# Optimization experiments

Hardware: AMD Instinct MI355X
Metric: run time of the kernel (lower is better)

Reference implementation:

```python
import jax, jax.numpy as jnp
import numpy as np

B, T, D = 4, 4096, 1024
H, K, V = 16, 64, 64
EPS = 1e-6


def setup_inputs() -> dict:
    key = jax.random.key(0)
    ks = jax.random.split(key, 7)
    s = 0.02
    return {
        "x": jax.random.normal(ks[0], (B, T, D), dtype=jnp.float32),
        "norm_w": jnp.ones((D,), dtype=jnp.float32),
        "Wk": jax.random.normal(ks[1], (H * K, D), dtype=jnp.float32) * s,
        "Wv": jax.random.normal(ks[2], (H * V, D), dtype=jnp.float32) * s,
        "Wo": jax.random.normal(ks[3], (D, H * V), dtype=jnp.float32) * s,
        "Wb": jax.random.normal(ks[4], (H, D), dtype=jnp.float32) * s,
        "bb": jnp.full((H,), -2.0, dtype=jnp.float32),
        "Wg": jax.random.normal(ks[5], (H, D), dtype=jnp.float32) * s,
        "bg": jnp.full((H,), 2.0, dtype=jnp.float32),
    }


def reference(x, norm_w, Wk, Wv, Wo, Wb, bb, Wg, bg):
    # RMSNorm
    rms = jnp.sqrt(jnp.mean(x * x, axis=-1, keepdims=True) + EPS)
    xn = x / rms * norm_w  # [B,T,D]

    k = (xn @ Wk.T).reshape(B, T, H, K)
    v = (xn @ Wv.T).reshape(B, T, H, V)
    # L2-normalize keys (F.normalize, eps=1e-12)
    kn = jnp.linalg.norm(k, axis=-1, keepdims=True)
    k = k / jnp.maximum(kn, 1e-12)

    beta = jax.nn.sigmoid(xn @ Wb.T + bb)  # [B,T,H]
    g = jax.nn.sigmoid(xn @ Wg.T + bg)     # [B,T,H]

    # time-major for scan
    k_t = jnp.transpose(k, (1, 0, 2, 3))       # [T,B,H,K]
    v_t = jnpp = jnp.transpose(v, (1, 0, 2, 3))  # [T,B,H,V]
    b_t = jnp.transpose(beta, (1, 0, 2))       # [T,B,H]
    g_t = jnp.transpose(g, (1, 0, 2))          # [T,B,H]

    state0 = jnp.zeros((B, H, K, V), dtype=jnp.float32)

    def step(state, inp):
        kt, vt, bt, gt = inp  # [B,H,K],[B,H,V],[B,H],[B,H]
        pred = jnp.einsum('bhkv,bhk->bhv', state, kt)
        err = vt - pred
        state = gt[..., None, None] * state + bt[..., None, None] * (kt[..., :, None] * err[..., None, :])
        out_t = jnp.einsum('bhkv,bhk->bhv', state, kt)
        return state, out_t

    final_state, out = jax.lax.scan(step, state0, (k_t, v_t, b_t, g_t))
    out = jnp.transpose(out, (1, 0, 2, 3)).reshape(B, T, H * V)  # [B,T,H*V]
    y = x + out @ Wo.T
    return y
```

## Files before the change

kernel.cpp:

```cpp
#include <hip/hip_runtime.h>
#include <stdint.h>

#define B_ 4
#define T_ 4096
#define D_ 1024
#define H_ 16
#define NPAD 2304
#define ROWS (B_*T_)

typedef __bf16 bf16x8 __attribute__((ext_vector_type(8)));
typedef float  f32x4  __attribute__((ext_vector_type(4)));
typedef unsigned short u16;
typedef u16 u16x8 __attribute__((ext_vector_type(8)));
typedef u16 u16x4 __attribute__((ext_vector_type(4)));

__device__ __forceinline__ float bf2f(u16 u){
  union { unsigned int i; float f; } x; x.i = ((unsigned int)u) << 16; return x.f;
}
__device__ __forceinline__ u16 f2bf(float f){
  union { float f; unsigned int i; } x; x.f = f;
  unsigned int r = x.i + 0x7fffu + ((x.i >> 16) & 1u);
  return (u16)(r >> 16);
}
__device__ __forceinline__ bf16x8 as_bf(u16x8 v){ union{u16x8 u; bf16x8 b;} x; x.u = v; return x.b; }

__device__ __forceinline__ void gload_lds16(const u16* g, u16* l){
  __builtin_amdgcn_global_load_lds(
      (const __attribute__((address_space(1))) unsigned int*)g,
      (__attribute__((address_space(3))) unsigned int*)l, 16, 0, 0);
}

__global__ __launch_bounds__(256) void prep_w(
    const float* __restrict__ Wk, const float* __restrict__ Wv,
    const float* __restrict__ Wb, const float* __restrict__ Wg,
    const float* __restrict__ Wo, u16* __restrict__ Wcomb, u16* __restrict__ Wob)
{
  long i = (long)blockIdx.x * 256 + threadIdx.x;
  const long tot1 = (long)NPAD * D_;
  if (i < tot1) {
    long n = i >> 10, d = i & 1023;
    float v;
    if      (n < 1024) v = Wk[n * 1024 + d];
    else if (n < 2048) v = Wv[(n - 1024) * 1024 + d];
    else if (n < 2064) v = Wb[(n - 2048) * 1024 + d];
    else if (n < 2080) v = Wg[(n - 2064) * 1024 + d];
    else               v = 0.f;
    Wcomb[i] = f2bf(v);
  } else {
    long j = i - tot1;
    Wob[j] = f2bf(Wo[j]);
  }
}

__global__ __launch_bounds__(256) void rmsnorm_k(
    const float* __restrict__ x, const float* __restrict__ w, u16* __restrict__ xn)
{
  long row = blockIdx.x;
  int tid = threadIdx.x;
  int l = tid & 63, wv = tid >> 6;
  f32x4 v = ((const f32x4*)(x + row * D_))[tid];
  float ss = v[0]*v[0] + v[1]*v[1] + v[2]*v[2] + v[3]*v[3];
  #pragma unroll
  for (int m = 1; m < 64; m <<= 1) ss += __shfl_xor(ss, m, 64);
  __shared__ float red[4];
  if (l == 0) red[wv] = ss;
  __syncthreads();
  float tot = red[0] + red[1] + red[2] + red[3];
  float inv = rsqrtf(tot * (1.f / (float)D_) + 1e-6f);
  f32x4 wv4 = ((const f32x4*)w)[tid];
  u16x4 o;
  o[0] = f2bf(v[0] * inv * wv4[0]);
  o[1] = f2bf(v[1] * inv * wv4[1]);
  o[2] = f2bf(v[2] * inv * wv4[2]);
  o[3] = f2bf(v[3] * inv * wv4[3]);
  ((u16x4*)(xn + row * D_))[tid] = o;
}

extern __shared__ f32x4 lds_dyn[];

template<int RESID, int OUTF32>
__global__ __launch_bounds__(512, 2) void gemm256(
    const u16* __restrict__ A, const u16* __restrict__ Bm,
    u16* __restrict__ Cb, float* __restrict__ Cf, const float* __restrict__ resid,
    int M, int N, int Kd)
{
  const int tid = threadIdx.x;
  const int w = tid >> 6, l = tid & 63;
  const int lm = l & 15, lq = l >> 4;
  const int wm = w >> 2, wn = w & 3;

  unsigned gx = gridDim.x;
  unsigned bid = blockIdx.y * gx + blockIdx.x;
  unsigned nwg = gx * gridDim.y;
  unsigned cpx = nwg >> 3;
  unsigned swz = (bid & 7) * cpx + (bid >> 3);
  const long bm0 = (long)(swz / gx) * 256;
  const long bn0 = (long)(swz % gx) * 256;

  char* lds = (char*)lds_dyn;

  int rowS[2];
  #pragma unroll
  for (int r = 0; r < 2; ++r) rowS[r] = r*128 + w*16 + (l >> 2);
  const int colS = ((l & 3) ^ ((l >> 3) & 3)) * 8;

  auto STAGE = [&](int t, int q){
    char* base = lds + q*32768;
    long k0 = (long)t * 32;
    #pragma unroll
    for (int r = 0; r < 2; ++r)
      gload_lds16(A + (bm0 + rowS[r])*(long)Kd + k0 + colS,
                  (u16*)(base + (r*512 + w*64)*16));
    #pragma unroll
    for (int r = 0; r < 2; ++r)
      gload_lds16(Bm + (bn0 + rowS[r])*(long)Kd + k0 + colS,
                  (u16*)(base + 16384 + (r*512 + w*64)*16));
  };

  const unsigned soff = (unsigned)(lq ^ ((lm >> 1) & 3)) << 4;

  f32x4 acc[8][4];
  #pragma unroll
  for (int i = 0; i < 8; ++i)
    #pragma unroll
    for (int j = 0; j < 4; ++j) acc[i][j] = f32x4{0.f,0.f,0.f,0.f};

  const int NT = Kd >> 5;
  STAGE(0, 0);
  STAGE(1, 1);
  STAGE(2, 2);

  for (int t = 0; t < NT; ++t) {
    int q  = t & 3;
    int qn = (t + 3) & 3;
    int tn = (t + 3 < NT) ? (t + 3) : (NT - 1);

    asm volatile("s_waitcnt vmcnt(8)" ::: "memory");
    __builtin_amdgcn_s_barrier();
    asm volatile("" ::: "memory");

    STAGE(tn, qn);

    const char* Ab = lds + q*32768;
    const char* Bb = Ab + 16384;

    bf16x8 bfr[4], afr[8];
    #pragma unroll
    for (int nf = 0; nf < 4; ++nf) {
      int rr = wn*64 + nf*16 + lm;
      bfr[nf] = *(const bf16x8*)(Bb + rr*64 + soff);
    }
    #pragma unroll
    for (int mf = 0; mf < 8; ++mf) {
      int rr = wm*128 + mf*16 + lm;
      afr[mf] = *(const bf16x8*)(Ab + rr*64 + soff);
    }

    __builtin_amdgcn_s_setprio(1);
    #pragma unroll
    for (int mf = 0; mf < 8; ++mf)
      #pragma unroll
      for (int nf = 0; nf < 4; ++nf)
        acc[mf][nf] = __builtin_amdgcn_mfma_f32_16x16x32_bf16(afr[mf], bfr[nf], acc[mf][nf], 0, 0, 0);
    __builtin_amdgcn_s_setprio(0);
  }

  #pragma unroll
  for (int mf = 0; mf < 8; ++mf) {
    #pragma unroll
    for (int r = 0; r < 4; ++r) {
      long m = bm0 + wm*128 + mf*16 + lq*4 + r;
      #pragma unroll
      for (int nf = 0; nf < 4; ++nf) {
        long n = bn0 + wn*64 + nf*16 + lm;
        float val = acc[mf][nf][r];
        if (RESID) val += resid[m * N + n];
        if (OUTF32) Cf[m * N + n] = val;
        else        Cb[m * N + n] = f2bf(val);
      }
    }
  }
}

template<int RESID, int OUTF32>
__global__ __launch_bounds__(256) void gemm_nt(
    const u16* __restrict__ A, const u16* __restrict__ Bm,
    u16* __restrict__ Cb, float* __restrict__ Cf, const float* __restrict__ resid,
    int M, int N, int Kd)
{
  __shared__ __align__(16) u16 Als[128 * 32];
  __shared__ __align__(16) u16 Bls[128 * 32];
  const int tid = threadIdx.x;
  const int w = tid >> 6, l = tid & 63;
  const int wr = w >> 1, wc = w & 1;
  const int lm = l & 15, lq = l >> 4;

  unsigned bid = blockIdx.y * gridDim.x + blockIdx.x;
  unsigned nwg = gridDim.x * gridDim.y;
  unsigned cpx = nwg >> 3;
  unsigned swz = (bid & 7) * cpx + (bid >> 3);
  const long bm0 = (long)(swz / gridDim.x) * 128;
  const long bn0 = (long)(swz % gridDim.x) * 128;

  f32x4 zero4 = {0.f, 0.f, 0.f, 0.f};
  f32x4 acc[4][4];
  #pragma unroll
  for (int i = 0; i < 4; i++)
    #pragma unroll
    for (int j = 0; j < 4; j++) acc[i][j] = zero4;

  for (int kk = 0; kk < Kd; kk += 32) {
    __syncthreads();
    #pragma unroll
    for (int it = 0; it < 2; it++) {
      int c = tid + it * 256;
      int r = c >> 2, kb = c & 3;
      const u16* ga = A  + (bm0 + r) * Kd + kk + kb * 8;
      const u16* gb = Bm + (bn0 + r) * Kd + kk + kb * 8;
      gload_lds16(ga, Als + (it * 256 + w * 64) * 8);
      gload_lds16(gb, Bls + (it * 256 + w * 64) * 8);
    }
    __syncthreads();
    bf16x8 af[4], bfr[4];
    #pragma unroll
    for (int f = 0; f < 4; f++)
      af[f] = *(const bf16x8*)(Als + (wr * 64 + f * 16 + lm) * 32 + lq * 8);
    #pragma unroll
    for (int f = 0; f < 4; f++)
      bfr[f] = *(const bf16x8*)(Bls + (wc * 64 + f * 16 + lm) * 32 + lq * 8);
    #pragma unroll
    for (int i = 0; i < 4; i++)
      #pragma unroll
      for (int j = 0; j < 4; j++)
        acc[i][j] = __builtin_amdgcn_mfma_f32_16x16x32_bf16(af[i], bfr[j], acc[i][j], 0, 0, 0);
  }

  #pragma unroll
  for (int i = 0; i < 4; i++) {
    #pragma unroll
    for (int r = 0; r < 4; r++) {
      long m = bm0 + wr * 64 + i * 16 + lq * 4 + r;
      #pragma unroll
      for (int j = 0; j < 4; j++) {
        long n = bn0 + wc * 64 + j * 16 + lm;
        float val = acc[i][j][r];
        if (RESID) val += resid[m * N + n];
        if (OUTF32) Cf[m * N + n] = val;
        else        Cb[m * N + n] = f2bf(val);
      }
    }
  }
}

__global__ __launch_bounds__(256) void sigmoid_bg(
    const u16* __restrict__ kv, const float* __restrict__ bb, const float* __restrict__ bg,
    float* __restrict__ bArr, float* __restrict__ gArr)
{
  int idx = blockIdx.x * 256 + threadIdx.x;
  int row = idx >> 5, c = idx & 31;
  int h = c & 15;
  float val = bf2f(kv[(long)row * NPAD + 2048 + c]) + ((c < 16) ? bb[h] : bg[h]);
  float s = 1.f / (1.f + expf(-val));
  long b = row >> 12, t = row & 4095;
  float* dst = (c < 16) ? bArr : gArr;
  dst[(b * H_ + h) * (long)T_ + t] = s;
}

__device__ __forceinline__ void mm64(const u16* Ab, const u16* Bb,
                                     int lm, int lq, int wr, int wc, f32x4 acc[2][2])
{
  #pragma unroll
  for (int ks = 0; ks < 2; ++ks) {
    bf16x8 af[2], bfr[2];
    #pragma unroll
    for (int mi = 0; mi < 2; ++mi)
      af[mi] = *(const bf16x8*)(Ab + (wr*32 + mi*16 + lm)*72 + ks*32 + lq*8);
    #pragma unroll
    for (int ni = 0; ni < 2; ++ni)
      bfr[ni] = *(const bf16x8*)(Bb + (wc*32 + ni*16 + lm)*72 + ks*32 + lq*8);
    #pragma unroll
    for (int mi = 0; mi < 2; ++mi)
      #pragma unroll
      for (int ni = 0; ni < 2; ++ni)
        acc[mi][ni] = __builtin_amdgcn_mfma_f32_16x16x32_bf16(af[mi], bfr[ni], acc[mi][ni], 0, 0, 0);
  }
}

__global__ __launch_bounds__(256) void chunk1(
    u16* __restrict__ kv, const float* __restrict__ bArr, const float* __restrict__ gArr,
    u16* __restrict__ p1buf, u16* __restrict__ r1buf)
{
  __shared__ __align__(16) u16 Kb[64*72];
  __shared__ __align__(16) u16 Utb[128*72];
  __shared__ __align__(16) u16 LpI[64*72];
  __shared__ __align__(16) u16 Abf[64*72];
  __shared__ __align__(16) u16 Adb[4*16*24];
  __shared__ float nrm2LS[64];
  __shared__ float aLS[64], ainvLS[64], bLS[64], bapLS[64];
  __shared__ float aCsh;

  const int tid = threadIdx.x;
  const int w = tid >> 6, l = tid & 63;
  const int lm = l & 15, lq = l >> 4;
  const int wr = w >> 1, wc = w & 1;
  const int bh = blockIdx.x & 63, ch = blockIdx.x >> 6;
  const int b = bh >> 4, h = bh & 15;

  const u16* kbase = kv + ((long)b*T_ + ch*64)*NPAD + h*64;
  const u16* vbase = kbase + 1024;

  #pragma unroll
  for (int it = 0; it < 2; ++it) {
    int c = tid + it*256;
    int r = c >> 3, seg = (c & 7)*8;
    *(u16x8*)(Kb  + r*72 + seg) = *(const u16x8*)(kbase + (long)r*NPAD + seg);
    *(u16x8*)(Utb + r*72 + seg) = *(const u16x8*)(vbase + (long)r*NPAD + seg);
  }
  #pragma unroll
  for (int z = 0; z < 8; ++z) {
    int idx = tid + z*256;
    int rr = idx >> 5, wd = idx & 31;
    ((unsigned int*)(Utb + (64 + rr)*72))[wd] = 0u;
  }
  if (tid < 64) {
    float gv = gArr[(long)bh*T_ + ch*64 + tid];
    float bv = bArr[(long)bh*T_ + ch*64 + tid];
    float av = gv;
    #pragma unroll
    for (int off = 1; off < 64; off <<= 1) {
      float o = __shfl_up(av, off, 64);
      if (tid >= off) av *= o;
    }
    float ap = __shfl_up(av, 1, 64);
    if (tid == 0) ap = 1.f;
    float aC = __shfl(av, 63, 64);
    aLS[tid] = av; ainvLS[tid] = 1.f/av; bLS[tid] = bv; bapLS[tid] = bv*ap;
    if (tid == 0) aCsh = aC;
  }
  __syncthreads();

  f32x4 gf[2][2];
  #pragma unroll
  for (int mi = 0; mi < 2; ++mi)
    #pragma unroll
    for (int ni = 0; ni < 2; ++ni) gf[mi][ni] = f32x4{0.f,0.f,0.f,0.f};
  mm64(Kb, Kb, lm, lq, wr, wc, gf);

  #pragma unroll
  for (int mi = 0; mi < 2; ++mi)
    #pragma unroll
    for (int ni = 0; ni < 2; ++ni)
      #pragma unroll
      for (int r = 0; r < 4; ++r) {
        int row = wr*32 + mi*16 + lq*4 + r, col = wc*32 + ni*16 + lm;
        if (row == col) nrm2LS[row] = gf[mi][ni][r];
      }
  __syncthreads();
  if (tid < 64) {
    float nv = 1.f / fmaxf(sqrtf(nrm2LS[tid]), 1e-12f);
    aLS[tid] *= nv; ainvLS[tid] *= nv; bapLS[tid] *= nv;
  }
  __syncthreads();

  float wv_[4][2][4];
  #pragma unroll
  for (int bi = 0; bi < 4; ++bi)
    #pragma unroll
    for (int ni = 0; ni < 2; ++ni) {
      int col = w*32 + ni*16 + lm;
      #pragma unroll
      for (int r = 0; r < 4; ++r) {
        int row = bi*16 + lq*4 + r;
        float sv = (col < 64) ? bf2f(Utb[row*72 + col]) : bf2f(Kb[row*72 + (col - 64)]);
        float coef = (col < 64) ? bLS[row] : bapLS[row];
        wv_[bi][ni][r] = coef * sv;
      }
    }

  #pragma unroll
  for (int mi = 0; mi < 2; ++mi)
    #pragma unroll
    for (int ni = 0; ni < 2; ++ni)
      #pragma unroll
      for (int r = 0; r < 4; ++r) {
        int row = wr*32 + mi*16 + lq*4 + r, col = wc*32 + ni*16 + lm;
        float gvl = gf[mi][ni][r];
        int rb = row >> 4, cb = col >> 4;
        Abf[row*72 + col] = f2bf((rb > cb) ? bapLS[row]*ainvLS[col]*gvl : 0.f);
        if (rb == cb)
          Adb[rb*384 + (row & 15)*24 + (col & 15)] =
              f2bf(((col & 15) < (row & 15)) ? bapLS[row]*ainvLS[col]*gvl : 0.f);
        LpI[row*72 + col] = f2bf((col < row) ? aLS[row]*ainvLS[col]*gvl
                                             : ((col == row) ? 1.f : 0.f));
      }
  __syncthreads();

  #pragma unroll
  for (int bi = 0; bi < 4; ++bi) {
    if (bi > 0) {
      f32x4 corr[2] = { f32x4{0.f,0.f,0.f,0.f}, f32x4{0.f,0.f,0.f,0.f} };
      const int nks = (bi*16 + 31) >> 5;
      #pragma unroll
      for (int ks = 0; ks < 2; ++ks) {
        if (ks < nks) {
          bf16x8 afr = *(const bf16x8*)(Abf + (bi*16 + lm)*72 + ks*32 + lq*8);
          #pragma unroll
          for (int ni = 0; ni < 2; ++ni) {
            bf16x8 bfr = *(const bf16x8*)(Utb + (w*32 + ni*16 + lm)*72 + ks*32 + lq*8);
            corr[ni] = __builtin_amdgcn_mfma_f32_16x16x32_bf16(afr, bfr, corr[ni], 0, 0, 0);
          }
        }
      }
      #pragma unroll
      for (int ni = 0; ni < 2; ++ni)
        #pragma unroll
        for (int r = 0; r < 4; ++r) wv_[bi][ni][r] -= corr[ni][r];
    }
    u16x8 ad0[4], ad1[4];
    #pragma unroll
    for (int r = 0; r < 4; ++r) {
      ad0[r] = *(const u16x8*)(Adb + bi*384 + (lq*4 + r)*24);
      ad1[r] = *(const u16x8*)(Adb + bi*384 + (lq*4 + r)*24 + 8);
    }
    #pragma unroll
    for (int i = 0; i < 16; ++i) {
      int src = ((i >> 2) << 4) | lm;
      float u0 = __shfl(wv_[bi][0][i & 3], src, 64);
      float u1 = __shfl(wv_[bi][1][i & 3], src, 64);
      #pragma unroll
      for (int r = 0; r < 4; ++r) {
        float ad = bf2f((i < 8) ? ad0[r][i] : ad1[r][i - 8]);
        wv_[bi][0][r] = fmaf(-ad, u0, wv_[bi][0][r]);
        wv_[bi][1][r] = fmaf(-ad, u1, wv_[bi][1][r]);
      }
    }
    #pragma unroll
    for (int ni = 0; ni < 2; ++ni) {
      int col = w*32 + ni*16 + lm;
      #pragma unroll
      for (int r = 0; r < 4; ++r)
        Utb[col*72 + bi*16 + lq*4 + r] = f2bf(wv_[bi][ni][r]);
    }
  }
  __syncthreads();

  const long pr_base = (((long)bh*64 + ch)*64);
  u16* qdst = kv + ((long)b*T_ + ch*64)*NPAD + h*64;
  u16* mdst = qdst + 1024;
  f32x4 acc[2][2];

  #pragma unroll
  for (int mi = 0; mi < 2; ++mi)
    #pragma unroll
    for (int ni = 0; ni < 2; ++ni) acc[mi][ni] = f32x4{0.f,0.f,0.f,0.f};
  mm64(Utb, LpI, lm, lq, wr, wc, acc);
  #pragma unroll
  for (int mi = 0; mi < 2; ++mi)
    #pragma unroll
    for (int ni = 0; ni < 2; ++ni)
      #pragma unroll
      for (int r = 0; r < 4; ++r) {
        int row = wr*32 + mi*16 + lq*4 + r, col = wc*32 + ni*16 + lm;
        p1buf[(pr_base + row)*64 + col] = f2bf(acc[mi][ni][r]);
      }

  #pragma unroll
  for (int mi = 0; mi < 2; ++mi)
    #pragma unroll
    for (int ni = 0; ni < 2; ++ni) acc[mi][ni] = f32x4{0.f,0.f,0.f,0.f};
  mm64(LpI, Utb + 64*72, lm, lq, wr, wc, acc);
  #pragma unroll
  for (int mi = 0; mi < 2; ++mi)
    #pragma unroll
    for (int ni = 0; ni < 2; ++ni)
      #pragma unroll
      for (int r = 0; r < 4; ++r) {
        int row = wr*32 + mi*16 + lq*4 + r, col = wc*32 + ni*16 + lm;
        float val = aLS[row]*bf2f(Kb[row*72 + col]) - acc[mi][ni][r];
        qdst[(long)row*NPAD + col] = f2bf(val);
      }

  {
    int s = tid & 63, kk0 = (tid >> 6) * 16;
    float coef = aCsh * ainvLS[s];
    #pragma unroll
    for (int j = 0; j < 16; ++j)
      Abf[(kk0 + j)*72 + s] = f2bf(coef * bf2f(Kb[s*72 + kk0 + j]));
  }
  __syncthreads();

  #pragma unroll
  for (int mi = 0; mi < 2; ++mi)
    #pragma unroll
    for (int ni = 0; ni < 2; ++ni) acc[mi][ni] = f32x4{0.f,0.f,0.f,0.f};
  mm64(Utb, Abf, lm, lq, wr, wc, acc);
  #pragma unroll
  for (int mi = 0; mi < 2; ++mi)
    #pragma unroll
    for (int ni = 0; ni < 2; ++ni)
      #pragma unroll
      for (int r = 0; r < 4; ++r) {
        int row = wr*32 + mi*16 + lq*4 + r, col = wc*32 + ni*16 + lm;
        r1buf[(pr_base + row)*64 + col] = f2bf(acc[mi][ni][r]);
      }

  #pragma unroll
  for (int mi = 0; mi < 2; ++mi)
    #pragma unroll
    for (int ni = 0; ni < 2; ++ni) acc[mi][ni] = f32x4{0.f,0.f,0.f,0.f};
  mm64(Abf, Utb + 64*72, lm, lq, wr, wc, acc);
  #pragma unroll
  for (int mi = 0; mi < 2; ++mi)
    #pragma unroll
    for (int ni = 0; ni < 2; ++ni)
      #pragma unroll
      for (int r = 0; r < 4; ++r) {
        int row = wr*32 + mi*16 + lq*4 + r, col = wc*32 + ni*16 + lm;
        float val = ((row == col) ? aCsh : 0.f) - acc[mi][ni][r];
        mdst[(long)row*NPAD + col] = f2bf(val);
      }
}

struct PF { u16x8 qf0, qf1, mf0, mf1; u16 p1[4]; u16 r1[4]; };

__global__ __launch_bounds__(256) void chunk2(
    const u16* __restrict__ kv, const u16* __restrict__ p1buf, const u16* __restrict__ r1buf,
    u16* __restrict__ outb)
{
  __shared__ __align__(16) u16 Zb[16*72];
  __shared__ __align__(16) u16 ot[64*24];
  const int tid = threadIdx.x;
  const int wcv = tid >> 6, l = tid & 63;
  const int lm = l & 15, lq = l >> 4;
  const int bh = blockIdx.x & 63, vg = blockIdx.x >> 6;
  const int b = bh >> 4, h = bh & 15;

  for (int idx = tid; idx < 16*72/2; idx += 256) ((unsigned int*)Zb)[idx] = 0u;

  const u16* pbase = p1buf + (long)bh*64*4096;
  const u16* rbase = r1buf + (long)bh*64*4096;

  auto LOADPF = [&](int ch, PF& p){
    long rq = ((long)b*T_ + ch*64 + wcv*16 + lm)*NPAD + h*64 + lq*8;
    p.qf0 = *(const u16x8*)(kv + rq);
    p.qf1 = *(const u16x8*)(kv + rq + 32);
    p.mf0 = *(const u16x8*)(kv + rq + 1024);
    p.mf1 = *(const u16x8*)(kv + rq + 1024 + 32);
    #pragma unroll
    for (int r = 0; r < 4; ++r) {
      long pv = (long)ch*4096 + (vg*16 + lq*4 + r)*64 + wcv*16 + lm;
      p.p1[r] = pbase[pv];
      p.r1[r] = rbase[pv];
    }
  };

  PF A, Bp;
  LOADPF(0, A);
  __syncthreads();

  auto STEP = [&](int ch, PF& use, PF& pre){
    bf16x8 za0 = *(const bf16x8*)(Zb + lm*72 + lq*8);
    bf16x8 za1 = *(const bf16x8*)(Zb + lm*72 + 32 + lq*8);
    if (ch < 63) LOADPF(ch + 1, pre);
    f32x4 accO = { bf2f(use.p1[0]), bf2f(use.p1[1]), bf2f(use.p1[2]), bf2f(use.p1[3]) };
    accO = __builtin_amdgcn_mfma_f32_16x16x32_bf16(za0, as_bf(use.qf0), accO, 0, 0, 0);
    accO = __builtin_amdgcn_mfma_f32_16x16x32_bf16(za1, as_bf(use.qf1), accO, 0, 0, 0);
    f32x4 accS = { bf2f(use.r1[0]), bf2f(use.r1[1]), bf2f(use.r1[2]), bf2f(use.r1[3]) };
    accS = __builtin_amdgcn_mfma_f32_16x16x32_bf16(za0, as_bf(use.mf0), accS, 0, 0, 0);
    accS = __builtin_amdgcn_mfma_f32_16x16x32_bf16(za1, as_bf(use.mf1), accS, 0, 0, 0);
    #pragma unroll
    for (int r = 0; r < 4; ++r) ot[(wcv*16 + lm)*24 + lq*4 + r] = f2bf(accO[r]);
    __syncthreads();
    #pragma unroll
    for (int r = 0; r < 4; ++r) Zb[(lq*4 + r)*72 + wcv*16 + lm] = f2bf(accS[r]);
    {
      int i2 = tid >> 2, q4 = tid & 3;
      u16x4 ov = *(const u16x4*)(ot + i2*24 + q4*4);
      *(u16x4*)(outb + ((long)b*T_ + ch*64 + i2)*D_ + h*64 + vg*16 + q4*4) = ov;
    }
    __syncthreads();
  };

  for (int c2 = 0; c2 < 32; ++c2) {
    STEP(2*c2,     A, Bp);
    STEP(2*c2 + 1, Bp, A);
  }
}

extern "C" void kernel_launch(void* const* d_in, const int* in_sizes, int n_in,
                              void* d_out, int out_size, void* d_ws, size_t ws_size,
                              hipStream_t stream) {
  const float* x     = (const float*)d_in[0];
  const float* normw = (const float*)d_in[1];
  const float* Wk    = (const float*)d_in[2];
  const float* Wv    = (const float*)d_in[3];
  const float* Wo    = (const float*)d_in[4];
  const float* Wb    = (const float*)d_in[5];
  const float* bb    = (const float*)d_in[6];
  const float* Wg    = (const float*)d_in[7];
  const float* bg    = (const float*)d_in[8];
  float* y = (float*)d_out;

  char* ws = (char*)d_ws;
  u16* xn    = (u16*)ws;   ws += (long)ROWS * D_ * 2;
  u16* Wcomb = (u16*)ws;   ws += (long)NPAD * D_ * 2;
  u16* Wob   = (u16*)ws;   ws += (long)D_ * D_ * 2;
  u16* kvb   = (u16*)ws;   ws += (long)ROWS * NPAD * 2;
  float* bA  = (float*)ws; ws += (long)B_ * H_ * T_ * 4;
  float* gA  = (float*)ws; ws += (long)B_ * H_ * T_ * 4;
  u16* outb  = (u16*)ws;   ws += (long)ROWS * D_ * 2;
  u16* r1b   = (u16*)ws;   ws += (long)64 * 64 * 4096 * 2;

  const int LDSB = 4 * 32768;
  bool big = true;
  if (hipFuncSetAttribute(reinterpret_cast<const void*>(gemm256<0,0>),
        hipFuncAttributeMaxDynamicSharedMemorySize, LDSB) != hipSuccess) big = false;
  if (hipFuncSetAttribute(reinterpret_cast<const void*>(gemm256<1,1>),
        hipFuncAttributeMaxDynamicSharedMemorySize, LDSB) != hipSuccess) big = false;

  const long prep_total = (long)NPAD * D_ + (long)D_ * D_;
  prep_w<<<dim3((unsigned)(prep_total / 256)), dim3(256), 0, stream>>>(
      Wk, Wv, Wb, Wg, Wo, Wcomb, Wob);
  rmsnorm_k<<<dim3(ROWS), dim3(256), 0, stream>>>(x, normw, xn);
  if (big)
    gemm256<0, 0><<<dim3(NPAD / 256, ROWS / 256), dim3(512), LDSB, stream>>>(
        xn, Wcomb, kvb, (float*)nullptr, (const float*)nullptr, ROWS, NPAD, D_);
  else
    gemm_nt<0, 0><<<dim3(NPAD / 128, ROWS / 128), dim3(256), 0, stream>>>(
        xn, Wcomb, kvb, (float*)nullptr, (const float*)nullptr, ROWS, NPAD, D_);
  sigmoid_bg<<<dim3(ROWS * 32 / 256), dim3(256), 0, stream>>>(kvb, bb, bg, bA, gA);
  chunk1<<<dim3(4096), dim3(256), 0, stream>>>(kvb, bA, gA, xn, r1b);
  chunk2<<<dim3(256), dim3(256), 0, stream>>>(kvb, xn, r1b, outb);
  if (big)
    gemm256<1, 1><<<dim3(D_ / 256, ROWS / 256), dim3(512), LDSB, stream>>>(
        outb, Wob, (u16*)nullptr, y, x, ROWS, D_, D_);
  else
    gemm_nt<1, 1><<<dim3(D_ / 128, ROWS / 128), dim3(256), 0, stream>>>(
        outb, Wob, (u16*)nullptr, y, x, ROWS, D_, D_);
}
```

Before: 323.3 us.

## Restructure 256x256 GEMM into 8-phase ping-pong pipeline with K=64 tiles

Replaces the 4-stage K=32 GEMM main loop with a double-buffered K=64 scheme. Each iteration is split into four MFMA quadrant phases, and the global-to-LDS loads for the next tiles are spread across those phases. Barriers, s_waitcnt and sched_barrier control the interleaving, and the LDS layout uses a new 128-byte row XOR swizzle. The goal is better overlap of memory loads, LDS reads and MFMA work in both projection GEMMs, at the cost of more barriers and a fragile hand-scheduled wait count.

```diff
diff --git a/kernel.cpp b/kernel.cpp
--- a/kernel.cpp
+++ b/kernel.cpp
@@ -78,8 +78,20 @@
 
 extern __shared__ f32x4 lds_dyn[];
 
+#define MMQ(AF, BF, MO, NO) \
+  __builtin_amdgcn_s_setprio(1); \
+  _Pragma("unroll") \
+  for (int mi = 0; mi < 4; ++mi) \
+    _Pragma("unroll") \
+    for (int ni = 0; ni < 2; ++ni) \
+      _Pragma("unroll") \
+      for (int ks = 0; ks < 2; ++ks) \
+        acc[(MO)+mi][(NO)+ni] = __builtin_amdgcn_mfma_f32_16x16x32_bf16( \
+            AF[mi][ks], BF[ni][ks], acc[(MO)+mi][(NO)+ni], 0, 0, 0); \
+  __builtin_amdgcn_s_setprio(0);
+
 template<int RESID, int OUTF32>
-__global__ __launch_bounds__(512, 2) void gemm256(
+__global__ __launch_bounds__(512, 2) void gemm8p(
     const u16* __restrict__ A, const u16* __restrict__ Bm,
     u16* __restrict__ Cb, float* __restrict__ Cf, const float* __restrict__ resid,
     int M, int N, int Kd)
@@ -98,26 +110,46 @@
   const long bn0 = (long)(swz % gx) * 256;
 
   char* lds = (char*)lds_dyn;
-
-  int rowS[2];
-  #pragma unroll
-  for (int r = 0; r < 2; ++r) rowS[r] = r*128 + w*16 + (l >> 2);
-  const int colS = ((l & 3) ^ ((l >> 3) & 3)) * 8;
-
-  auto STAGE = [&](int t, int q){
-    char* base = lds + q*32768;
-    long k0 = (long)t * 32;
-    #pragma unroll
-    for (int r = 0; r < 2; ++r)
-      gload_lds16(A + (bm0 + rowS[r])*(long)Kd + k0 + colS,
-                  (u16*)(base + (r*512 + w*64)*16));
-    #pragma unroll
-    for (int r = 0; r < 2; ++r)
-      gload_lds16(Bm + (bn0 + rowS[r])*(long)Kd + k0 + colS,
-                  (u16*)(base + 16384 + (r*512 + w*64)*16));
+  const int NTS = Kd >> 6;
+
+  auto STAGE_AU = [&](int t, int rowBase){
+    if (t >= NTS) return;
+    char* base = lds + (t & 1) * 65536;
+    int c = w*64 + l;
+    int row = rowBase + (c >> 3);
+    int kc = (c & 7) ^ (row & 7);
+    gload_lds16(A + (bm0 + row)*(long)Kd + (long)t*64 + kc*8,
+                (u16*)(base + rowBase*128 + c*16));
   };
-
-  const unsigned soff = (unsigned)(lq ^ ((lm >> 1) & 3)) << 4;
+  auto STAGE_BU = [&](int t, int sb){
+    if (t >= NTS) return;
+    char* base = lds + (t & 1) * 65536 + 32768;
+    int stripeBase = sb + (w >> 2) * 64;
+    int ci = (w & 3)*64 + l;
+    int row = stripeBase + (ci >> 3);
+    int kc = (ci & 7) ^ (row & 7);
+    gload_lds16(Bm + (bn0 + row)*(long)Kd + (long)t*64 + kc*8,
+                (u16*)(base + stripeBase*128 + (w & 3)*1024 + l*16));
+  };
+
+  auto RD_A = [&](const char* Ab, int qm, bf16x8 afr[4][2]){
+    #pragma unroll
+    for (int mi = 0; mi < 4; ++mi) {
+      int rr = wm*128 + qm*64 + mi*16 + lm;
+      #pragma unroll
+      for (int ks = 0; ks < 2; ++ks)
+        afr[mi][ks] = *(const bf16x8*)(Ab + rr*128 + ((ks*64 + lq*16) ^ ((rr & 7) << 4)));
+    }
+  };
+  auto RD_B = [&](const char* Bb, int qn, bf16x8 bfr[2][2]){
+    #pragma unroll
+    for (int ni = 0; ni < 2; ++ni) {
+      int rr = wn*64 + qn*32 + ni*16 + lm;
+      #pragma unroll
+      for (int ks = 0; ks < 2; ++ks)
+        bfr[ni][ks] = *(const bf16x8*)(Bb + rr*128 + ((ks*64 + lq*16) ^ ((rr & 7) << 4)));
+    }
+  };
 
   f32x4 acc[8][4];
   #pragma unroll
@@ -125,44 +157,54 @@
     #pragma unroll
     for (int j = 0; j < 4; ++j) acc[i][j] = f32x4{0.f,0.f,0.f,0.f};
 
-  const int NT = Kd >> 5;
-  STAGE(0, 0);
-  STAGE(1, 1);
-  STAGE(2, 2);
-
-  for (int t = 0; t < NT; ++t) {
-    int q  = t & 3;
-    int qn = (t + 3) & 3;
-    int tn = (t + 3 < NT) ? (t + 3) : (NT - 1);
-
-    asm volatile("s_waitcnt vmcnt(8)" ::: "memory");
-    __builtin_amdgcn_s_barrier();
-    asm volatile("" ::: "memory");
-
-    STAGE(tn, qn);
-
-    const char* Ab = lds + q*32768;
-    const char* Bb = Ab + 16384;
-
-    bf16x8 bfr[4], afr[8];
-    #pragma unroll
-    for (int nf = 0; nf < 4; ++nf) {
-      int rr = wn*64 + nf*16 + lm;
-      bfr[nf] = *(const bf16x8*)(Bb + rr*64 + soff);
-    }
-    #pragma unroll
-    for (int mf = 0; mf < 8; ++mf) {
-      int rr = wm*128 + mf*16 + lm;
-      afr[mf] = *(const bf16x8*)(Ab + rr*64 + soff);
-    }
-
-    __builtin_amdgcn_s_setprio(1);
-    #pragma unroll
-    for (int mf = 0; mf < 8; ++mf)
-      #pragma unroll
-      for (int nf = 0; nf < 4; ++nf)
-        acc[mf][nf] = __builtin_amdgcn_mfma_f32_16x16x32_bf16(afr[mf], bfr[nf], acc[mf][nf], 0, 0, 0);
-    __builtin_amdgcn_s_setprio(0);
+  bf16x8 afr0[4][2], afr1[4][2], bfr[2][2];
+
+  STAGE_AU(0, 0);   STAGE_AU(0, 128); STAGE_BU(0, 0);  STAGE_BU(0, 128);
+  STAGE_AU(0, 64);  STAGE_AU(0, 192); STAGE_BU(0, 32); STAGE_BU(0, 160);
+  STAGE_AU(1, 0);   STAGE_AU(1, 128); STAGE_BU(1, 0);  STAGE_BU(1, 128);
+  STAGE_AU(1, 64);  STAGE_AU(1, 192); STAGE_BU(1, 32);
+  asm volatile("s_waitcnt vmcnt(7)" ::: "memory");
+  __builtin_amdgcn_s_barrier();
+
+  for (int t = 0; t < NTS; ++t) {
+    const char* Ab = lds + (t & 1) * 65536;
+    const char* Bb = Ab + 32768;
+
+    asm volatile("s_waitcnt vmcnt(7)" ::: "memory");
+    RD_A(Ab, 0, afr0);
+    RD_B(Bb, 0, bfr);
+    STAGE_BU(t + 1, 160);
+    __builtin_amdgcn_s_barrier();
+    asm volatile("s_waitcnt lgkmcnt(0)" ::: "memory");
+    __builtin_amdgcn_sched_barrier(0);
+    MMQ(afr0, bfr, 0, 0);
+    __builtin_amdgcn_s_barrier();
+
+    RD_A(Ab, 1, afr1);
+    STAGE_AU(t + 2, 0);
+    __builtin_amdgcn_s_barrier();
+    asm volatile("s_waitcnt lgkmcnt(0)" ::: "memory");
+    __builtin_amdgcn_sched_barrier(0);
+    MMQ(afr1, bfr, 4, 0);
+    __builtin_amdgcn_s_barrier();
+
+    RD_B(Bb, 1, bfr);
+    STAGE_AU(t + 2, 128);
+    STAGE_BU(t + 2, 0);
+    STAGE_AU(t + 2, 64);
+    __builtin_amdgcn_s_barrier();
+    asm volatile("s_waitcnt lgkmcnt(0)" ::: "memory");
+    __builtin_amdgcn_sched_barrier(0);
+    MMQ(afr1, bfr, 4, 2);
+    __builtin_amdgcn_s_barrier();
+
+    asm volatile("s_waitcnt vmcnt(5)" ::: "memory");
+    STAGE_BU(t + 2, 128);
+    STAGE_AU(t + 2, 192);
+    STAGE_BU(t + 2, 32);
+    __builtin_amdgcn_s_barrier();
+    MMQ(afr0, bfr, 0, 2);
+    __builtin_amdgcn_s_barrier();
   }
 
   #pragma unroll
@@ -406,8 +448,8 @@
           bf16x8 afr = *(const bf16x8*)(Abf + (bi*16 + lm)*72 + ks*32 + lq*8);
           #pragma unroll
           for (int ni = 0; ni < 2; ++ni) {
-            bf16x8 bfr = *(const bf16x8*)(Utb + (w*32 + ni*16 + lm)*72 + ks*32 + lq*8);
-            corr[ni] = __builtin_amdgcn_mfma_f32_16x16x32_bf16(afr, bfr, corr[ni], 0, 0, 0);
+            bf16x8 bfrv = *(const bf16x8*)(Utb + (w*32 + ni*16 + lm)*72 + ks*32 + lq*8);
+            corr[ni] = __builtin_amdgcn_mfma_f32_16x16x32_bf16(afr, bfrv, corr[ni], 0, 0, 0);
           }
         }
       }
@@ -611,11 +653,11 @@
   u16* outb  = (u16*)ws;   ws += (long)ROWS * D_ * 2;
   u16* r1b   = (u16*)ws;   ws += (long)64 * 64 * 4096 * 2;
 
-  const int LDSB = 4 * 32768;
+  const int LDSB = 2 * 65536;
   bool big = true;
-  if (hipFuncSetAttribute(reinterpret_cast<const void*>(gemm256<0,0>),
+  if (hipFuncSetAttribute(reinterpret_cast<const void*>(gemm8p<0,0>),
         hipFuncAttributeMaxDynamicSharedMemorySize, LDSB) != hipSuccess) big = false;
-  if (hipFuncSetAttribute(reinterpret_cast<const void*>(gemm256<1,1>),
+  if (hipFuncSetAttribute(reinterpret_cast<const void*>(gemm8p<1,1>),
         hipFuncAttributeMaxDynamicSharedMemorySize, LDSB) != hipSuccess) big = false;
 
   const long prep_total = (long)NPAD * D_ + (long)D_ * D_;
@@ -623,7 +665,7 @@
       Wk, Wv, Wb, Wg, Wo, Wcomb, Wob);
   rmsnorm_k<<<dim3(ROWS), dim3(256), 0, stream>>>(x, normw, xn);
   if (big)
-    gemm256<0, 0><<<dim3(NPAD / 256, ROWS / 256), dim3(512), LDSB, stream>>>(
+    gemm8p<0, 0><<<dim3(NPAD / 256, ROWS / 256), dim3(512), LDSB, stream>>>(
         xn, Wcomb, kvb, (float*)nullptr, (const float*)nullptr, ROWS, NPAD, D_);
   else
     gemm_nt<0, 0><<<dim3(NPAD / 128, ROWS / 128), dim3(256), 0, stream>>>(
@@ -632,7 +674,7 @@
   chunk1<<<dim3(4096), dim3(256), 0, stream>>>(kvb, bA, gA, xn, r1b);
   chunk2<<<dim3(256), dim3(256), 0, stream>>>(kvb, xn, r1b, outb);
   if (big)
-    gemm256<1, 1><<<dim3(D_ / 256, ROWS / 256), dim3(512), LDSB, stream>>>(
+    gemm8p<1, 1><<<dim3(D_ / 256, ROWS / 256), dim3(512), LDSB, stream>>>(
         outb, Wob, (u16*)nullptr, y, x, ROWS, D_, D_);
   else
     gemm_nt<1, 1><<<dim3(D_ / 128, ROWS / 128), dim3(256), 0, stream>>>(
```

Result: faster. 310.9 us (-3.8%).
